# Kernel tuning notes

Measured on AMD Instinct MI355X. Metric: run time of the kernel, lower is better.

## Reference

```python
import jax, jax.numpy as jnp
import numpy as np

B, L, H = 2, 4096, 1024
ED, N, R, K = 2048, 16, 64, 4


def setup_inputs() -> dict:
    key = jax.random.key(0)
    ks = jax.random.split(key, 8)
    w = lambda i, shape, s=0.02: jax.random.normal(ks[i], shape, jnp.float32) * s
    # dt bias initialized like Mamba: inv-softplus of dt ~ logU(1e-3, 1e-1)
    dt = jnp.exp(jax.random.uniform(ks[7], (ED,)) * (np.log(0.1) - np.log(0.001)) + np.log(0.001))
    dt = jnp.clip(dt, 1e-4)
    inv_dt = dt + jnp.log(-jnp.expm1(-dt))
    A = jnp.broadcast_to(jnp.arange(1, N + 1, dtype=jnp.float32), (ED, N))
    return dict(
        x=jax.random.normal(ks[0], (B, L, H), jnp.float32),
        in_proj_w=w(1, (2 * ED, H)),
        conv_w=w(2, (ED, K), 0.2),
        conv_b=jnp.zeros((ED,), jnp.float32),
        x_proj_w=w(3, (R + 2 * N, ED)),
        dt_w=w(4, (ED, R), 64 ** -0.5),
        dt_b=inv_dt,
        A_log=jnp.log(A),
        D=jnp.ones((ED,), jnp.float32),
        out_proj_w=w(5, (H, ED)),
    )


def reference(x, in_proj_w, conv_w, conv_b, x_proj_w, dt_w, dt_b, A_log, D, out_proj_w):
    Bq, Lq, Hq = x.shape
    EDq, Kq = conv_w.shape
    Rq = dt_w.shape[1]
    Nq = A_log.shape[1]

    # in_proj -> [B, L, 2*ED]; chunk into hidden_states and gate
    xz = jnp.einsum('blh,eh->ble', x, in_proj_w)
    hs, gate = jnp.split(xz, 2, axis=-1)

    # causal depthwise conv1d along L (padding K-1 on the left), then SiLU
    hs_pad = jnp.pad(hs, ((0, 0), (Kq - 1, 0), (0, 0)))  # [B, L+K-1, ED]
    conv = conv_b
    for k in range(Kq):  # K=4, fixed small loop
        conv = conv + hs_pad[:, k:k + Lq, :] * conv_w[:, k]
    hs = jax.nn.silu(conv)  # [B, L, ED]

    # x_proj -> split into dt (rank R), B (N), C (N)
    ssm = jnp.einsum('ble,pe->blp', hs, x_proj_w)
    dtr, Bm, Cm = jnp.split(ssm, [Rq, Rq + Nq], axis=-1)

    # dt_proj + softplus (delta_softplus=True with delta_bias)
    delta = jax.nn.softplus(jnp.einsum('blr,er->ble', dtr, dt_w) + dt_b)  # [B,L,ED]

    A = -jnp.exp(A_log)  # [ED, N]

    # selective scan: h_t = exp(delta_t*A)*h_{t-1} + delta_t*B_t*u_t ; y_t = <h_t, C_t>
    def step(h, inp):
        d_t, B_t, C_t, u_t = inp  # [B,ED], [B,N], [B,N], [B,ED]
        dA = jnp.exp(d_t[..., None] * A)                      # [B,ED,N]
        h = dA * h + (d_t * u_t)[..., None] * B_t[:, None, :]  # [B,ED,N]
        y = jnp.einsum('ben,bn->be', h, C_t)                   # [B,ED]
        return h, y

    h0 = jnp.zeros((Bq, EDq, Nq), x.dtype)
    xs = (jnp.moveaxis(delta, 1, 0), jnp.moveaxis(Bm, 1, 0),
          jnp.moveaxis(Cm, 1, 0), jnp.moveaxis(hs, 1, 0))
    _, ys = jax.lax.scan(step, h0, xs)  # ys: [L, B, ED]

    y = jnp.moveaxis(ys, 0, 1) + hs * D      # skip term D*u
    y = y * jax.nn.silu(gate)                # gated output
    return jnp.einsum('ble,he->blh', y, out_proj_w)
```

## Files before the change

### kernel.cpp

```cpp
#include <hip/hip_runtime.h>


typedef float f32x4 __attribute__((ext_vector_type(4)));
typedef short short8 __attribute__((ext_vector_type(8)));

#define DEV __device__ __forceinline__

DEV float bf2f(unsigned short u) {
  union { unsigned int i; float f; } v; v.i = ((unsigned int)u) << 16; return v.f;
}
DEV unsigned short f2bf(float f) {
  union { float f; unsigned int i; } v; v.f = f;
  return (unsigned short)((v.i + 0x7fffu + ((v.i >> 16) & 1u)) >> 16);
}

DEV void gload_lds16(const void* g, void* l) {
  __builtin_amdgcn_global_load_lds(
      (const __attribute__((address_space(1))) unsigned int*)g,
      (__attribute__((address_space(3))) unsigned int*)l, 16, 0, 0);
}

DEV void mfma_bf16(f32x4& d, short8 a, short8 b) {
  asm("v_mfma_f32_16x16x32_bf16 %0, %1, %2, %0" : "+v"(d) : "v"(a), "v"(b));
}

template <int BM, int BN, int WM, int WN, int EPI>
__global__ __launch_bounds__(256) void gemm_bt_kernel(
    const unsigned short* __restrict__ A, const unsigned short* __restrict__ Bw,
    int M, int N, int Kd,
    float* __restrict__ o_f32, unsigned short* __restrict__ o_b16a,
    unsigned short* __restrict__ o_b16b, const float* __restrict__ bias,
    float* __restrict__ oB, float* __restrict__ oC)
{
  constexpr int MFR = BM / WM / 16;
  constexpr int NFR = BN / WN / 16;
  constexpr int TA = BM * 4;
  constexpr int TB = BN * 4;
  __shared__ unsigned short lds[(BM + BN) * 32];

  const int tid  = threadIdx.x;
  const int wave = tid >> 6;
  const int lane = tid & 63;
  const int row  = lane & 15;
  const int g    = lane >> 4;
  const int swz  = g ^ ((row >> 1) & 3);
  const int rowBase = blockIdx.y * BM;
  const int colBase = blockIdx.x * BN;
  const int WROW = (wave / WN) * (BM / WM);
  const int WCOL = (wave % WN) * (BN / WN);

  f32x4 acc[MFR][NFR];
  const f32x4 fz = {0.f, 0.f, 0.f, 0.f};
#pragma unroll
  for (int i = 0; i < MFR; ++i)
#pragma unroll
    for (int j = 0; j < NFR; ++j) acc[i][j] = fz;

  for (int kk = 0; kk < Kd; kk += 32) {
#pragma unroll
    for (int c0 = 0; c0 < TA; c0 += 256) {
      int ch = c0 + tid;
      if (ch < TA) {
        int r = ch >> 2;
        int gs = (ch & 3) ^ ((r >> 1) & 3);
        gload_lds16(A + (size_t)(rowBase + r) * Kd + kk + gs * 8,
                    (void*)(lds + (c0 + wave * 64) * 8));
      }
    }
#pragma unroll
    for (int c0 = 0; c0 < TB; c0 += 256) {
      int ch = c0 + tid;
      if (ch < TB) {
        int r = ch >> 2;
        int gs = (ch & 3) ^ ((r >> 1) & 3);
        gload_lds16(Bw + (size_t)(colBase + r) * Kd + kk + gs * 8,
                    (void*)(lds + BM * 32 + (c0 + wave * 64) * 8));
      }
    }
    __syncthreads();
    short8 af[MFR], bfr[NFR];
#pragma unroll
    for (int mi = 0; mi < MFR; ++mi)
      af[mi] = *(const short8*)(lds + (WROW + mi * 16 + row) * 32 + swz * 8);
#pragma unroll
    for (int ni = 0; ni < NFR; ++ni)
      bfr[ni] = *(const short8*)(lds + BM * 32 + (WCOL + ni * 16 + row) * 32 + swz * 8);
#pragma unroll
    for (int mi = 0; mi < MFR; ++mi)
#pragma unroll
      for (int ni = 0; ni < NFR; ++ni)
        mfma_bf16(acc[mi][ni], af[mi], bfr[ni]);
    __syncthreads();
  }

#pragma unroll
  for (int mi = 0; mi < MFR; ++mi) {
#pragma unroll
    for (int ni = 0; ni < NFR; ++ni) {
      const int gcol = colBase + WCOL + ni * 16 + row;
#pragma unroll
      for (int r = 0; r < 4; ++r) {
        const int grow = rowBase + WROW + mi * 16 + g * 4 + r;
        float v = acc[mi][ni][r];
        if constexpr (EPI == 0) {
          o_f32[(size_t)grow * N + gcol] = v;
        } else if constexpr (EPI == 1) {
          if (gcol < 2048) o_b16a[(size_t)grow * 2048 + gcol] = f2bf(v);
          else             o_b16b[(size_t)grow * 2048 + (gcol - 2048)] = f2bf(v);
        } else if constexpr (EPI == 2) {
          if (gcol < 64)      o_b16a[(size_t)grow * 64 + gcol] = f2bf(v);
          else if (gcol < 80) oB[(size_t)grow * 16 + (gcol - 64)] = v;
          else                oC[(size_t)grow * 16 + (gcol - 80)] = v;
        } else {
          float x = v + bias[gcol];
          o_f32[(size_t)grow * N + gcol] = (x > 20.f) ? x : __logf(1.f + __expf(x));
        }
      }
    }
  }
}

__global__ __launch_bounds__(256) void cvt_bf16_kernel(
    const float* __restrict__ in, unsigned short* __restrict__ out, int n8)
{
  int i = blockIdx.x * 256 + threadIdx.x;
  if (i >= n8) return;
  const float4* p = (const float4*)(in + (size_t)i * 8);
  float4 a = p[0], b = p[1];
  float v[8] = {a.x, a.y, a.z, a.w, b.x, b.y, b.z, b.w};
  unsigned o[4];
#pragma unroll
  for (int q = 0; q < 4; ++q)
    o[q] = (unsigned)f2bf(v[2 * q]) | ((unsigned)f2bf(v[2 * q + 1]) << 16);
  *(uint4*)(out + (size_t)i * 8) = make_uint4(o[0], o[1], o[2], o[3]);
}

__global__ __launch_bounds__(256) void conv_silu_kernel(
    const unsigned short* __restrict__ hsraw, const float* __restrict__ cw,
    const float* __restrict__ cb, unsigned short* __restrict__ hsb)
{
  int idx = blockIdx.x * 256 + threadIdx.x;
  int e0 = (idx & 255) * 8;
  int t  = (idx >> 8) & 4095;
  int b  = idx >> 20;
  float acc[8];
  float wv[4][8];
#pragma unroll
  for (int j = 0; j < 8; ++j) acc[j] = cb[e0 + j];
#pragma unroll
  for (int k = 0; k < 4; ++k)
#pragma unroll
    for (int j = 0; j < 8; ++j) wv[k][j] = cw[(e0 + j) * 4 + k];
#pragma unroll
  for (int k = 0; k < 4; ++k) {
    int tt = t - 3 + k;
    if (tt < 0) continue;
    uint4 v4 = *(const uint4*)(hsraw + ((size_t)(b * 4096 + tt)) * 2048 + e0);
    unsigned arr[4] = {v4.x, v4.y, v4.z, v4.w};
#pragma unroll
    for (int q = 0; q < 4; ++q) {
      acc[2 * q]     += wv[k][2 * q]     * bf2f((unsigned short)(arr[q] & 0xffffu));
      acc[2 * q + 1] += wv[k][2 * q + 1] * bf2f((unsigned short)(arr[q] >> 16));
    }
  }
  unsigned o[4];
#pragma unroll
  for (int q = 0; q < 4; ++q) {
    float a0 = acc[2 * q], a1 = acc[2 * q + 1];
    a0 = a0 / (1.f + __expf(-a0));
    a1 = a1 / (1.f + __expf(-a1));
    o[q] = (unsigned)f2bf(a0) | ((unsigned)f2bf(a1) << 16);
  }
  *(uint4*)(hsb + ((size_t)(b * 4096 + t)) * 2048 + e0) = make_uint4(o[0], o[1], o[2], o[3]);
}

__global__ __launch_bounds__(256) void scan_phase1(
    const float* __restrict__ delta, const unsigned short* __restrict__ hsb,
    const float* __restrict__ Bb, const float* __restrict__ alog,
    float* __restrict__ h_end, float* __restrict__ Ssum)
{
  __shared__ __align__(16) float Bs[64 * 16];
  const int tid = threadIdx.x;
  const int e = blockIdx.x * 256 + tid;
  const int c = blockIdx.y;
  const int b = blockIdx.z;
  const int t0 = c * 64;
  {
    const float* src = Bb + ((size_t)(b * 4096 + t0)) * 16;
#pragma unroll
    for (int k = 0; k < 4; ++k) Bs[tid + k * 256] = src[tid + k * 256];
  }
  float An[16];
  {
    const float4* ap = (const float4*)(alog + e * 16);
#pragma unroll
    for (int q = 0; q < 4; ++q) {
      float4 v = ap[q];
      An[4*q+0] = -__expf(v.x); An[4*q+1] = -__expf(v.y);
      An[4*q+2] = -__expf(v.z); An[4*q+3] = -__expf(v.w);
    }
  }
  __syncthreads();
  float h[16];
#pragma unroll
  for (int n = 0; n < 16; ++n) h[n] = 0.f;
  float sumd = 0.f;
  size_t base = ((size_t)(b * 4096 + t0)) * 2048 + e;
  float dd = delta[base];
  float uu = bf2f(hsb[base]);
  for (int j = 0; j < 64; ++j) {
    int jn = (j < 63) ? j + 1 : 63;
    float d_nxt = delta[base + (size_t)jn * 2048];
    float u_nxt = bf2f(hsb[base + (size_t)jn * 2048]);
    const float4* Bv = (const float4*)(Bs + j * 16);
    float4 b0 = Bv[0], b1 = Bv[1], b2 = Bv[2], b3 = Bv[3];
    float Bl[16] = {b0.x,b0.y,b0.z,b0.w, b1.x,b1.y,b1.z,b1.w,
                    b2.x,b2.y,b2.z,b2.w, b3.x,b3.y,b3.z,b3.w};
    sumd += dd;
    float du = dd * uu;
#pragma unroll
    for (int n = 0; n < 16; ++n)
      h[n] = fmaf(__expf(An[n] * dd), h[n], du * Bl[n]);
    dd = d_nxt; uu = u_nxt;
  }
  float* he = h_end + (((size_t)(b * 2048 + e)) * 64 + c) * 16;
#pragma unroll
  for (int q = 0; q < 4; ++q) {
    float4 v = {h[4*q], h[4*q+1], h[4*q+2], h[4*q+3]};
    *(float4*)(he + 4 * q) = v;
  }
  Ssum[((size_t)(b * 2048 + e)) * 64 + c] = sumd;
}

__global__ __launch_bounds__(256) void scan_phase2(
    const float* __restrict__ h_end, const float* __restrict__ Ssum,
    const float* __restrict__ alog, float* __restrict__ h_start)
{
  const int tid = threadIdx.x;
  const int n = tid & 15;
  const int G = blockIdx.x * 16 + (tid >> 4);
  const int e = G & 2047;
  const float An = -__expf(alog[e * 16 + n]);
  size_t hb = (size_t)G * 64 * 16 + n;
  size_t sb = (size_t)G * 64;
  float h = 0.f;
  constexpr int PF = 8;
  float hq[PF], Sq[PF];
#pragma unroll
  for (int j = 0; j < PF; ++j) { hq[j] = h_end[hb + (size_t)j * 16]; Sq[j] = Ssum[sb + j]; }
  for (int c0 = 0; c0 < 64; c0 += PF) {
    float hn[PF], Sn[PF];
#pragma unroll
    for (int j = 0; j < PF; ++j) {
      int cn = c0 + PF + j; cn = (cn < 64) ? cn : 63;
      hn[j] = h_end[hb + (size_t)cn * 16]; Sn[j] = Ssum[sb + cn];
    }
#pragma unroll
    for (int j = 0; j < PF; ++j) {
      h_start[hb + (size_t)(c0 + j) * 16] = h;
      h = fmaf(__expf(An * Sq[j]), h, hq[j]);
    }
#pragma unroll
    for (int j = 0; j < PF; ++j) { hq[j] = hn[j]; Sq[j] = Sn[j]; }
  }
}

__global__ __launch_bounds__(256) void scan_phase3(
    const float* __restrict__ delta, const unsigned short* __restrict__ hsb,
    const float* __restrict__ Bb, const float* __restrict__ Cb,
    const float* __restrict__ alog, const float* __restrict__ h_start,
    const float* __restrict__ Dv, unsigned short* __restrict__ gate_y2)
{
  __shared__ __align__(16) float Bs[64 * 16];
  __shared__ __align__(16) float Cs[64 * 16];
  const int tid = threadIdx.x;
  const int e = blockIdx.x * 256 + tid;
  const int c = blockIdx.y;
  const int b = blockIdx.z;
  const int t0 = c * 64;
  {
    const float* srcB = Bb + ((size_t)(b * 4096 + t0)) * 16;
    const float* srcC = Cb + ((size_t)(b * 4096 + t0)) * 16;
#pragma unroll
    for (int k = 0; k < 4; ++k) {
      Bs[tid + k * 256] = srcB[tid + k * 256];
      Cs[tid + k * 256] = srcC[tid + k * 256];
    }
  }
  float An[16];
  {
    const float4* ap = (const float4*)(alog + e * 16);
#pragma unroll
    for (int q = 0; q < 4; ++q) {
      float4 v = ap[q];
      An[4*q+0] = -__expf(v.x); An[4*q+1] = -__expf(v.y);
      An[4*q+2] = -__expf(v.z); An[4*q+3] = -__expf(v.w);
    }
  }
  const float De = Dv[e];
  float h[16];
  {
    const float4* hp = (const float4*)(h_start + (((size_t)(b * 2048 + e)) * 64 + c) * 16);
#pragma unroll
    for (int q = 0; q < 4; ++q) {
      float4 v = hp[q];
      h[4*q+0] = v.x; h[4*q+1] = v.y; h[4*q+2] = v.z; h[4*q+3] = v.w;
    }
  }
  __syncthreads();
  size_t base = ((size_t)(b * 4096 + t0)) * 2048 + e;
  float dd = delta[base];
  float uu = bf2f(hsb[base]);
  float gg = bf2f(gate_y2[base]);
  for (int j = 0; j < 64; ++j) {
    int jn = (j < 63) ? j + 1 : 63;
    float d_nxt = delta[base + (size_t)jn * 2048];
    float u_nxt = bf2f(hsb[base + (size_t)jn * 2048]);
    float g_nxt = bf2f(gate_y2[base + (size_t)jn * 2048]);
    const float4* Bv = (const float4*)(Bs + j * 16);
    const float4* Cv = (const float4*)(Cs + j * 16);
    float4 b0 = Bv[0], b1 = Bv[1], b2 = Bv[2], b3 = Bv[3];
    float4 c0v = Cv[0], c1v = Cv[1], c2v = Cv[2], c3v = Cv[3];
    float Bl[16] = {b0.x,b0.y,b0.z,b0.w, b1.x,b1.y,b1.z,b1.w,
                    b2.x,b2.y,b2.z,b2.w, b3.x,b3.y,b3.z,b3.w};
    float Cl[16] = {c0v.x,c0v.y,c0v.z,c0v.w, c1v.x,c1v.y,c1v.z,c1v.w,
                    c2v.x,c2v.y,c2v.z,c2v.w, c3v.x,c3v.y,c3v.z,c3v.w};
    float du = dd * uu;
    float y = 0.f;
#pragma unroll
    for (int n = 0; n < 16; ++n) {
      h[n] = fmaf(__expf(An[n] * dd), h[n], du * Bl[n]);
      y = fmaf(h[n], Cl[n], y);
    }
    float val = (y + uu * De) * (gg / (1.f + __expf(-gg)));
    gate_y2[base + (size_t)j * 2048] = f2bf(val);
    dd = d_nxt; uu = u_nxt; gg = g_nxt;
  }
}

extern "C" void kernel_launch(void* const* d_in, const int* in_sizes, int n_in,
                              void* d_out, int out_size, void* d_ws, size_t ws_size,
                              hipStream_t stream)
{
  const float* x    = (const float*)d_in[0];
  const float* w1   = (const float*)d_in[1];
  const float* cw   = (const float*)d_in[2];
  const float* cb   = (const float*)d_in[3];
  const float* xp   = (const float*)d_in[4];
  const float* dtw  = (const float*)d_in[5];
  const float* dtb  = (const float*)d_in[6];
  const float* alog = (const float*)d_in[7];
  const float* Dp   = (const float*)d_in[8];
  const float* wo   = (const float*)d_in[9];
  float* out = (float*)d_out;
  char* ws = (char*)d_ws;

  const size_t o_xb    = 0;
  const size_t o_wb1   = 16777216;
  const size_t o_xpb   = 25165824;
  const size_t o_dtwb  = 25559040;
  const size_t o_wob   = 25821184;
  const size_t o_hsraw = 30015488;
  const size_t o_gate  = 63569920;
  const size_t o_hsb   = 97124352;
  const size_t o_dtrb  = 130678784;
  const size_t o_Bb    = 131727360;
  const size_t o_Cb    = 132251648;
  const size_t o_delta = 132775936;
  const size_t WS_NEED = o_delta + 67108864 + 262144;
  if (ws_size < WS_NEED) return;

  unsigned short* xb    = (unsigned short*)(ws + o_xb);
  unsigned short* wb1   = (unsigned short*)(ws + o_wb1);
  unsigned short* xpb   = (unsigned short*)(ws + o_xpb);
  unsigned short* dtwb  = (unsigned short*)(ws + o_dtwb);
  unsigned short* wob   = (unsigned short*)(ws + o_wob);
  unsigned short* hsraw = (unsigned short*)(ws + o_hsraw);
  unsigned short* gate  = (unsigned short*)(ws + o_gate);
  unsigned short* hsb   = (unsigned short*)(ws + o_hsb);
  unsigned short* dtrb  = (unsigned short*)(ws + o_dtrb);
  float* Bb    = (float*)(ws + o_Bb);
  float* Cb    = (float*)(ws + o_Cb);
  float* delta = (float*)(ws + o_delta);
  float* h_end   = (float*)(ws + o_xb);
  float* h_start = (float*)(ws + o_hsraw);
  float* Ssum    = (float*)(ws + o_hsraw + 16777216);

  cvt_bf16_kernel<<<4096, 256, 0, stream>>>(x,   xb,   1048576);
  cvt_bf16_kernel<<<2048, 256, 0, stream>>>(w1,  wb1,  524288);
  cvt_bf16_kernel<<<96,   256, 0, stream>>>(xp,  xpb,  24576);
  cvt_bf16_kernel<<<64,   256, 0, stream>>>(dtw, dtwb, 16384);
  cvt_bf16_kernel<<<1024, 256, 0, stream>>>(wo,  wob,  262144);

  gemm_bt_kernel<128,128,2,2,1><<<dim3(32,64), 256, 0, stream>>>(
      xb, wb1, 8192, 4096, 1024, nullptr, hsraw, gate, nullptr, nullptr, nullptr);
  conv_silu_kernel<<<8192, 256, 0, stream>>>(hsraw, cw, cb, hsb);
  gemm_bt_kernel<64,96,4,1,2><<<dim3(1,128), 256, 0, stream>>>(
      hsb, xpb, 8192, 96, 2048, nullptr, dtrb, nullptr, nullptr, Bb, Cb);
  gemm_bt_kernel<64,64,2,2,3><<<dim3(32,128), 256, 0, stream>>>(
      dtrb, dtwb, 8192, 2048, 64, delta, nullptr, nullptr, dtb, nullptr, nullptr);

  scan_phase1<<<dim3(8, 64, 2), 256, 0, stream>>>(delta, hsb, Bb, alog, h_end, Ssum);
  scan_phase2<<<256, 256, 0, stream>>>(h_end, Ssum, alog, h_start);
  scan_phase3<<<dim3(8, 64, 2), 256, 0, stream>>>(
      delta, hsb, Bb, Cb, alog, h_start, Dp, gate);

  gemm_bt_kernel<128,128,2,2,0><<<dim3(8,64), 256, 0, stream>>>(
      gate, wob, 8192, 1024, 2048, out, nullptr, nullptr, nullptr, nullptr, nullptr);
}
```

Baseline: 394.8 us.

## Triple-buffer GEMM LDS tiles with async prefetch and retile x_proj GEMM

```diff
diff --git a/kernel.cpp b/kernel.cpp
--- a/kernel.cpp
+++ b/kernel.cpp
@@ -22,6 +22,15 @@
 
 DEV void mfma_bf16(f32x4& d, short8 a, short8 b) {
   asm("v_mfma_f32_16x16x32_bf16 %0, %1, %2, %0" : "+v"(d) : "v"(a), "v"(b));
+}
+
+template <int N> DEV void wait_vmcnt() {
+  static_assert(N == 0 || N == 1 || N == 2 || N == 4 || N == 8, "unsupported");
+  if constexpr (N == 0)      asm volatile("s_waitcnt vmcnt(0)" ::: "memory");
+  else if constexpr (N == 1) asm volatile("s_waitcnt vmcnt(1)" ::: "memory");
+  else if constexpr (N == 2) asm volatile("s_waitcnt vmcnt(2)" ::: "memory");
+  else if constexpr (N == 4) asm volatile("s_waitcnt vmcnt(4)" ::: "memory");
+  else                       asm volatile("s_waitcnt vmcnt(8)" ::: "memory");
 }
 
 template <int BM, int BN, int WM, int WN, int EPI>
@@ -36,7 +45,11 @@
   constexpr int NFR = BN / WN / 16;
   constexpr int TA = BM * 4;
   constexpr int TB = BN * 4;
-  __shared__ unsigned short lds[(BM + BN) * 32];
+  constexpr int TILE = (BM + BN) * 32;
+  constexpr int LA3 = (TA > 192) ? ((TA - 193) / 256 + 1) : 0;
+  constexpr int LB3 = (TB > 192) ? ((TB - 193) / 256 + 1) : 0;
+  constexpr int LPS = LA3 + LB3;
+  __shared__ unsigned short lds[TILE * 3];
 
   const int tid  = threadIdx.x;
   const int wave = tid >> 6;
@@ -49,14 +62,8 @@
   const int WROW = (wave / WN) * (BM / WM);
   const int WCOL = (wave % WN) * (BN / WN);
 
-  f32x4 acc[MFR][NFR];
-  const f32x4 fz = {0.f, 0.f, 0.f, 0.f};
-#pragma unroll
-  for (int i = 0; i < MFR; ++i)
-#pragma unroll
-    for (int j = 0; j < NFR; ++j) acc[i][j] = fz;
-
-  for (int kk = 0; kk < Kd; kk += 32) {
+  auto stage = [&](int kt, int bufbase) {
+    const int kk = kt * 32;
 #pragma unroll
     for (int c0 = 0; c0 < TA; c0 += 256) {
       int ch = c0 + tid;
@@ -64,7 +71,7 @@
         int r = ch >> 2;
         int gs = (ch & 3) ^ ((r >> 1) & 3);
         gload_lds16(A + (size_t)(rowBase + r) * Kd + kk + gs * 8,
-                    (void*)(lds + (c0 + wave * 64) * 8));
+                    (void*)(lds + bufbase + (c0 + wave * 64) * 8));
       }
     }
 #pragma unroll
@@ -74,23 +81,51 @@
         int r = ch >> 2;
         int gs = (ch & 3) ^ ((r >> 1) & 3);
         gload_lds16(Bw + (size_t)(colBase + r) * Kd + kk + gs * 8,
-                    (void*)(lds + BM * 32 + (c0 + wave * 64) * 8));
+                    (void*)(lds + bufbase + BM * 32 + (c0 + wave * 64) * 8));
       }
     }
-    __syncthreads();
+  };
+
+  f32x4 acc[MFR][NFR];
+  const f32x4 fz = {0.f, 0.f, 0.f, 0.f};
+#pragma unroll
+  for (int i = 0; i < MFR; ++i)
+#pragma unroll
+    for (int j = 0; j < NFR; ++j) acc[i][j] = fz;
+
+  const int nt = Kd / 32;
+  stage(0, 0);
+  stage(1, TILE);
+  int cur = 0;
+  for (int t = 0; t < nt; ++t) {
+    if (t + 2 < nt) {
+      int b2 = cur + 2; if (b2 >= 3) b2 -= 3;
+      stage(t + 2, b2 * TILE);
+      wait_vmcnt<2 * LPS>();
+    } else if (t + 1 < nt) {
+      wait_vmcnt<LPS>();
+    } else {
+      wait_vmcnt<0>();
+    }
+    __builtin_amdgcn_sched_barrier(0);
+    __builtin_amdgcn_s_barrier();
+    __builtin_amdgcn_sched_barrier(0);
+    const unsigned short* lb = lds + cur * TILE;
     short8 af[MFR], bfr[NFR];
 #pragma unroll
     for (int mi = 0; mi < MFR; ++mi)
-      af[mi] = *(const short8*)(lds + (WROW + mi * 16 + row) * 32 + swz * 8);
+      af[mi] = *(const short8*)(lb + (WROW + mi * 16 + row) * 32 + swz * 8);
 #pragma unroll
     for (int ni = 0; ni < NFR; ++ni)
-      bfr[ni] = *(const short8*)(lds + BM * 32 + (WCOL + ni * 16 + row) * 32 + swz * 8);
+      bfr[ni] = *(const short8*)(lb + BM * 32 + (WCOL + ni * 16 + row) * 32 + swz * 8);
 #pragma unroll
     for (int mi = 0; mi < MFR; ++mi)
 #pragma unroll
       for (int ni = 0; ni < NFR; ++ni)
         mfma_bf16(acc[mi][ni], af[mi], bfr[ni]);
-    __syncthreads();
+    __builtin_amdgcn_sched_barrier(0);
+    __builtin_amdgcn_s_barrier();
+    cur += 1; if (cur >= 3) cur -= 3;
   }
 
 #pragma unroll
@@ -395,7 +430,7 @@
   gemm_bt_kernel<128,128,2,2,1><<<dim3(32,64), 256, 0, stream>>>(
       xb, wb1, 8192, 4096, 1024, nullptr, hsraw, gate, nullptr, nullptr, nullptr);
   conv_silu_kernel<<<8192, 256, 0, stream>>>(hsraw, cw, cb, hsb);
-  gemm_bt_kernel<64,96,4,1,2><<<dim3(1,128), 256, 0, stream>>>(
+  gemm_bt_kernel<32,96,2,2,2><<<dim3(1,256), 256, 0, stream>>>(
       hsb, xpb, 8192, 96, 2048, nullptr, dtrb, nullptr, nullptr, Bb, Cb);
   gemm_bt_kernel<64,64,2,2,3><<<dim3(32,128), 256, 0, stream>>>(
       dtrb, dtwb, 8192, 2048, 64, delta, nullptr, nullptr, dtb, nullptr, nullptr);
```

New measurement: 386.1 us. -2.2%, faster.
